# Kernel optimization log

Hardware: AMD Instinct MI355X
Metric: run time of the kernel (lower is better)

Reference implementation:

```python
import jax, jax.numpy as jnp
import numpy as np

NUM_HEADS = 16


def setup_inputs() -> dict:
    key = jax.random.key(0)
    k1, k2, k3, k4 = jax.random.split(key, 4)
    B, S, E = 2, 2048, 1024
    x = jax.random.normal(k1, (B, S, E), dtype=jnp.float32)
    src_padding_mask = jax.random.randint(k2, (B, S), 0, 2) > 0  # True = keep
    # xavier-uniform-ish scale for linear weights (shape (out, in), torch convention)
    w_qkv = jax.random.normal(k3, (3 * E, E), dtype=jnp.float32) * (1.0 / np.sqrt(E))
    w_o = jax.random.normal(k4, (E, E), dtype=jnp.float32) * (1.0 / np.sqrt(E))
    return {"x": x, "src_padding_mask": src_padding_mask, "w_qkv": w_qkv, "w_o": w_o}


def reference(x, src_padding_mask, w_qkv, w_o):
    B, S, E = x.shape
    H = NUM_HEADS
    D = E // H
    # fused qkv projection: (B,S,3E) -> (B,S,H,3D) -> split
    qkv = jnp.einsum("bse,fe->bsf", x, w_qkv).reshape(B, S, H, 3 * D)
    q, k, v = jnp.split(qkv, 3, axis=-1)
    # (B,H,S,D)
    q = q.transpose(0, 2, 1, 3)
    k = k.transpose(0, 2, 1, 3)
    v = v.transpose(0, 2, 1, 3)
    logits = jnp.einsum("bhqd,bhkd->bhqk", q, k) / jnp.sqrt(jnp.float32(D))
    logits = jnp.where(src_padding_mask[:, None, None, :], logits, -jnp.inf)
    attn = jax.nn.softmax(logits, axis=-1)
    values = jnp.einsum("bhqk,bhkd->bhqd", attn, v)  # (B,H,S,D)
    values = values.transpose(0, 2, 1, 3).reshape(B, S, E)
    out = jnp.einsum("bse,fe->bsf", values, w_o)
    return out
```

## Files before the change

kernel.cpp:

```cpp
#include <hip/hip_runtime.h>
#include <hip/hip_bf16.h>

#define B_NUM 2
#define S_LEN 2048
#define E_DIM 1024
#define H_NUM 16
#define D_DIM 64
#define QKV_LD 3072
#define QSCALE_LOG2E 0.18033688011112042f

typedef __attribute__((ext_vector_type(8))) short bf16x8;
typedef __attribute__((ext_vector_type(8))) unsigned short u16x8;
typedef __attribute__((ext_vector_type(4))) unsigned short u16x4;
typedef __attribute__((ext_vector_type(4))) float f32x4;
typedef __attribute__((ext_vector_type(16))) float f32x16;
typedef __attribute__((ext_vector_type(2))) int i32x2;

static __device__ __forceinline__ unsigned short f2bf(float f) {
    union { float f; unsigned int u; } v; v.f = f;
    unsigned int r = v.u + 0x7fffu + ((v.u >> 16) & 1u);
    return (unsigned short)(r >> 16);
}

static __device__ __forceinline__ float bf2f(unsigned short u) {
    union { unsigned int u; float f; } v; v.u = ((unsigned int)u) << 16;
    return v.f;
}

static __device__ __forceinline__ unsigned cvtpk_bf16(float lo, float hi) {
    unsigned r;
    asm("v_cvt_pk_bf16_f32 %0, %1, %2" : "=v"(r) : "v"(lo), "v"(hi));
    return r;
}

static __device__ __forceinline__ void gload16(const void* gsrc, void* ldst) {
    __builtin_amdgcn_global_load_lds(
        (const __attribute__((address_space(1))) unsigned int*)gsrc,
        (__attribute__((address_space(3))) unsigned int*)ldst, 16, 0, 0);
}

__global__ __launch_bounds__(256)
void cvt_f32_bf16(const float* __restrict__ in, unsigned short* __restrict__ outp, int n4) {
    int i = blockIdx.x * blockDim.x + threadIdx.x;
    if (i < n4) {
        float4 f = ((const float4*)in)[i];
        u16x4 o = { f2bf(f.x), f2bf(f.y), f2bf(f.z), f2bf(f.w) };
        ((u16x4*)outp)[i] = o;
    }
}

template <bool OUT_BF16, bool QSCALE>
__global__ __launch_bounds__(256)
void gemm_bt_mfma128(const unsigned short* __restrict__ A,
                     const unsigned short* __restrict__ Bw,
                     void* __restrict__ Cv, int M, int N, int K) {
    __shared__ unsigned short As[128 * 64];
    __shared__ unsigned short Bs[128 * 64];
    char* const AsB = (char*)As;
    char* const BsB = (char*)Bs;
    const int tid  = threadIdx.x;
    const int lane = tid & 63;
    const int w    = tid >> 6;
    const int lg   = lane >> 4;
    const int lq   = lane & 15;
    const int bm = blockIdx.y * 128;
    const int bn = blockIdx.x * 128;
    const int wr = (w >> 1) * 64;
    const int wc = (w & 1) * 64;
    const int lrow8 = lane >> 3;
    const int gblk  = (lane & 7) ^ lrow8;

    f32x4 acc[4][4];
#pragma unroll
    for (int i = 0; i < 4; ++i)
#pragma unroll
        for (int j = 0; j < 4; ++j) acc[i][j] = (f32x4){0.f, 0.f, 0.f, 0.f};

    for (int k0 = 0; k0 < K; k0 += 64) {
        __syncthreads();
#pragma unroll
        for (int t = 0; t < 4; ++t) {
            const int c = w * 4 + t;
            const int row = c * 8 + lrow8;
            gload16(A + (size_t)(bm + row) * K + k0 + gblk * 8, AsB + c * 1024);
            gload16(Bw + (size_t)(bn + row) * K + k0 + gblk * 8, BsB + c * 1024);
        }
        __syncthreads();

        bf16x8 af[4][2], bfr[4][2];
#pragma unroll
        for (int rt = 0; rt < 4; ++rt) {
            const int row = wr + rt * 16 + lq;
            const int sz = (row & 7) << 4;
            af[rt][0] = *(const bf16x8*)(AsB + row * 128 + ((lg * 16)      ^ sz));
            af[rt][1] = *(const bf16x8*)(AsB + row * 128 + ((64 + lg * 16) ^ sz));
        }
#pragma unroll
        for (int ct = 0; ct < 4; ++ct) {
            const int row = wc + ct * 16 + lq;
            const int sz = (row & 7) << 4;
            bfr[ct][0] = *(const bf16x8*)(BsB + row * 128 + ((lg * 16)      ^ sz));
            bfr[ct][1] = *(const bf16x8*)(BsB + row * 128 + ((64 + lg * 16) ^ sz));
        }
#pragma unroll
        for (int rt = 0; rt < 4; ++rt)
#pragma unroll
            for (int ct = 0; ct < 4; ++ct) {
                acc[rt][ct] = __builtin_amdgcn_mfma_f32_16x16x32_bf16(af[rt][0], bfr[ct][0], acc[rt][ct], 0, 0, 0);
                acc[rt][ct] = __builtin_amdgcn_mfma_f32_16x16x32_bf16(af[rt][1], bfr[ct][1], acc[rt][ct], 0, 0, 0);
            }
    }

#pragma unroll
    for (int rt = 0; rt < 4; ++rt)
#pragma unroll
        for (int ct = 0; ct < 4; ++ct) {
            const int row = bm + wr + rt * 16 + lg * 4;
            const int col = bn + wc + ct * 16 + lq;
            float scale = 1.f;
            if constexpr (QSCALE) scale = ((col % 192) < 64) ? QSCALE_LOG2E : 1.f;
#pragma unroll
            for (int r = 0; r < 4; ++r) {
                float vv = acc[rt][ct][r] * scale;
                if constexpr (OUT_BF16)
                    ((unsigned short*)Cv)[(size_t)(row + r) * N + col] = f2bf(vv);
                else
                    ((float*)Cv)[(size_t)(row + r) * N + col] = vv;
            }
        }
}

template <bool OUT_BF16, bool QSCALE>
__global__ __launch_bounds__(256)
void gemm_bt_mfma(const unsigned short* __restrict__ A,
                  const unsigned short* __restrict__ Bw,
                  void* __restrict__ Cv, int M, int N, int K) {
    __shared__ unsigned short As[64 * 64];
    __shared__ unsigned short Bs[64 * 64];
    char* const AsB = (char*)As;
    char* const BsB = (char*)Bs;
    const int tid  = threadIdx.x;
    const int lane = tid & 63;
    const int w    = tid >> 6;
    const int lg   = lane >> 4;
    const int lq   = lane & 15;
    const int bm = blockIdx.y * 64;
    const int bn = blockIdx.x * 64;
    const int wr = (w >> 1) * 32;
    const int wc = (w & 1) * 32;
    const int sr = tid >> 2;
    const int sc = (tid & 3) * 16;
    const int swzS = (sr & 7) << 4;

    f32x4 acc[2][2];
#pragma unroll
    for (int i = 0; i < 2; ++i)
#pragma unroll
        for (int j = 0; j < 2; ++j) acc[i][j] = (f32x4){0.f, 0.f, 0.f, 0.f};

    const unsigned short* ap = A  + (size_t)(bm + sr) * K + sc;
    const unsigned short* bp = Bw + (size_t)(bn + sr) * K + sc;

    for (int k0 = 0; k0 < K; k0 += 64) {
        __syncthreads();
        u16x8 av0 = *(const u16x8*)(ap + k0);
        u16x8 av1 = *(const u16x8*)(ap + k0 + 8);
        u16x8 bv0 = *(const u16x8*)(bp + k0);
        u16x8 bv1 = *(const u16x8*)(bp + k0 + 8);
        *(u16x8*)(AsB + sr * 128 + ((sc * 2)      ^ swzS)) = av0;
        *(u16x8*)(AsB + sr * 128 + ((sc * 2 + 16) ^ swzS)) = av1;
        *(u16x8*)(BsB + sr * 128 + ((sc * 2)      ^ swzS)) = bv0;
        *(u16x8*)(BsB + sr * 128 + ((sc * 2 + 16) ^ swzS)) = bv1;
        __syncthreads();

        bf16x8 af[2][2], bfr[2][2];
#pragma unroll
        for (int rt = 0; rt < 2; ++rt) {
            const int row = wr + rt * 16 + lq;
            const int sz = (row & 7) << 4;
            af[rt][0] = *(const bf16x8*)(AsB + row * 128 + ((lg * 16)      ^ sz));
            af[rt][1] = *(const bf16x8*)(AsB + row * 128 + ((64 + lg * 16) ^ sz));
        }
#pragma unroll
        for (int ct = 0; ct < 2; ++ct) {
            const int row = wc + ct * 16 + lq;
            const int sz = (row & 7) << 4;
            bfr[ct][0] = *(const bf16x8*)(BsB + row * 128 + ((lg * 16)      ^ sz));
            bfr[ct][1] = *(const bf16x8*)(BsB + row * 128 + ((64 + lg * 16) ^ sz));
        }
#pragma unroll
        for (int rt = 0; rt < 2; ++rt)
#pragma unroll
            for (int ct = 0; ct < 2; ++ct) {
                acc[rt][ct] = __builtin_amdgcn_mfma_f32_16x16x32_bf16(af[rt][0], bfr[ct][0], acc[rt][ct], 0, 0, 0);
                acc[rt][ct] = __builtin_amdgcn_mfma_f32_16x16x32_bf16(af[rt][1], bfr[ct][1], acc[rt][ct], 0, 0, 0);
            }
    }

#pragma unroll
    for (int rt = 0; rt < 2; ++rt)
#pragma unroll
        for (int ct = 0; ct < 2; ++ct) {
            const int row = bm + wr + rt * 16 + lg * 4;
            const int col = bn + wc + ct * 16 + lq;
            float scale = 1.f;
            if constexpr (QSCALE) scale = ((col % 192) < 64) ? QSCALE_LOG2E : 1.f;
#pragma unroll
            for (int r = 0; r < 4; ++r) {
                float vv = acc[rt][ct][r] * scale;
                if constexpr (OUT_BF16)
                    ((unsigned short*)Cv)[(size_t)(row + r) * N + col] = f2bf(vv);
                else
                    ((float*)Cv)[(size_t)(row + r) * N + col] = vv;
            }
        }
}

__global__ __launch_bounds__(256)
void attn_v14(const unsigned short* __restrict__ qkv, const int* __restrict__ mask,
              unsigned short* __restrict__ Po, float* __restrict__ Zp) {
    __shared__ __align__(16) char KsP[2][8192];
    __shared__ __align__(16) char VtP[2][8192];
    __shared__ __align__(16) float BiasF[1024];

    const int tid  = threadIdx.x;
    const int lane = tid & 63;
    const int w    = tid >> 6;
    const int ln   = lane & 31;
    const int hi   = lane >> 5;
    const int part = blockIdx.x & 1;
    const int q0   = (blockIdx.x >> 1) * 128;
    const int h  = blockIdx.y;
    const int b  = blockIdx.z;
    const int kvbase = part * 1024;
    const unsigned short* const kv =
        qkv + (size_t)b * S_LEN * QKV_LD + (size_t)h * (3 * D_DIM);

    {
        const int4* mr = (const int4*)(mask + (size_t)b * S_LEN + kvbase);
        int4 m0 = mr[tid];
        float4 f0 = { m0.x ? 0.f : -30000.f, m0.y ? 0.f : -30000.f,
                      m0.z ? 0.f : -30000.f, m0.w ? 0.f : -30000.f };
        ((float4*)BiasF)[tid] = f0;
    }

    bf16x8 qf[4];
    {
        const unsigned short* qp = kv + (size_t)(q0 + w * 32 + ln) * QKV_LD + hi * 8;
#pragma unroll
        for (int kk = 0; kk < 4; ++kk)
            qf[kk] = *(const bf16x8*)(qp + kk * 16);
    }

    const int lrow8 = lane >> 3;
    const int gblk  = (lane & 7) ^ lrow8;
    const int vkb = (tid & 15) * 4;
    const int vdb = (tid >> 4) * 4;

    {
#pragma unroll
        for (int t = 0; t < 2; ++t) {
            const int c = w * 2 + t;
            gload16(kv + (size_t)(kvbase + c * 8 + lrow8) * QKV_LD + D_DIM + gblk * 8,
                    KsP[0] + c * 1024);
        }
        u16x4 vr[4];
#pragma unroll
        for (int i = 0; i < 4; ++i)
            vr[i] = *(const u16x4*)(kv + (size_t)(kvbase + vkb + i) * QKV_LD + 2 * D_DIM + vdb);
#pragma unroll
        for (int j = 0; j < 4; ++j) {
            u16x4 o = { vr[0][j], vr[1][j], vr[2][j], vr[3][j] };
            const int row = vdb + j;
            *(u16x4*)(VtP[0] + row * 128 + ((vkb * 2) ^ ((row & 7) << 4))) = o;
        }
    }
    __syncthreads();

    f32x16 accO[2];
#pragma unroll
    for (int dt = 0; dt < 2; ++dt)
#pragma unroll
        for (int r = 0; r < 16; ++r) accO[dt][r] = 0.f;
    f32x4 rsumv = (f32x4){0.f, 0.f, 0.f, 0.f};

    const int NT = 16;
    for (int it = 0; it < NT; ++it) {
        const int cur = it & 1;
        const int kv0l = it * 64;
        const int kvg  = kvbase + it * 64;
        char* const KsC = KsP[cur];
        char* const VtC = VtP[cur];
        const bool pf = (it + 1 < NT);

        u16x4 vr[4];
        if (pf) {
            const int kvn = kvg + 64;
#pragma unroll
            for (int t = 0; t < 2; ++t) {
                const int c = w * 2 + t;
                gload16(kv + (size_t)(kvn + c * 8 + lrow8) * QKV_LD + D_DIM + gblk * 8,
                        KsP[cur ^ 1] + c * 1024);
            }
#pragma unroll
            for (int i = 0; i < 4; ++i)
                vr[i] = *(const u16x4*)(kv + (size_t)(kvn + vkb + i) * QKV_LD + 2 * D_DIM + vdb);
        }

        f32x16 s[2];
#pragma unroll
        for (int ks = 0; ks < 2; ++ks)
#pragma unroll
            for (int m = 0; m < 4; ++m) {
                f32x4 b4 = *(const f32x4*)(&BiasF[kv0l + ks * 32 + m * 8 + hi * 4]);
#pragma unroll
                for (int i = 0; i < 4; ++i) s[ks][m * 4 + i] = b4[i];
            }
        __builtin_amdgcn_s_setprio(1);
#pragma unroll
        for (int ks = 0; ks < 2; ++ks) {
            const int krow = ks * 32 + ln;
            const int swz = (ln & 7) << 4;
#pragma unroll
            for (int kk = 0; kk < 4; ++kk) {
                bf16x8 kf = *(const bf16x8*)(KsC + krow * 128 + (((kk * 16 + hi * 8) * 2) ^ swz));
                s[ks] = __builtin_amdgcn_mfma_f32_32x32x16_bf16(kf, qf[kk], s[ks], 0, 0, 0);
            }
        }
        __builtin_amdgcn_s_setprio(0);

#pragma unroll
        for (int ks = 0; ks < 2; ++ks)
#pragma unroll
            for (int r = 0; r < 16; ++r) {
                float p = __builtin_amdgcn_exp2f(s[ks][r]);
                s[ks][r] = p;
                rsumv[r & 3] += p;
            }

        bf16x8 pb[4];
#pragma unroll
        for (int ks = 0; ks < 2; ++ks) {
            unsigned wA[4], wB[4];
#pragma unroll
            for (int m = 0; m < 4; ++m) {
                wA[m] = cvtpk_bf16(s[ks][4 * m + 0], s[ks][4 * m + 1]);
                wB[m] = cvtpk_bf16(s[ks][4 * m + 2], s[ks][4 * m + 3]);
            }
#pragma unroll
            for (int t = 0; t < 2; ++t) {
                i32x2 ra = __builtin_amdgcn_permlane32_swap((int)wA[2 * t], (int)wA[2 * t + 1], false, false);
                i32x2 rb = __builtin_amdgcn_permlane32_swap((int)wB[2 * t], (int)wB[2 * t + 1], false, false);
                union { unsigned u[4]; bf16x8 v; } uu;
                uu.u[0] = (unsigned)ra[0];
                uu.u[1] = (unsigned)rb[0];
                uu.u[2] = (unsigned)ra[1];
                uu.u[3] = (unsigned)rb[1];
                pb[ks * 2 + t] = uu.v;
            }
        }

        __builtin_amdgcn_s_setprio(1);
#pragma unroll
        for (int dt = 0; dt < 2; ++dt) {
            const int drow = dt * 32 + ln;
            const int swz = (ln & 7) << 4;
#pragma unroll
            for (int n = 0; n < 4; ++n) {
                bf16x8 va = *(const bf16x8*)(VtC + drow * 128 + (((n * 16 + hi * 8) * 2) ^ swz));
                accO[dt] = __builtin_amdgcn_mfma_f32_32x32x16_bf16(va, pb[n], accO[dt], 0, 0, 0);
            }
        }
        __builtin_amdgcn_s_setprio(0);

        if (pf) {
#pragma unroll
            for (int j = 0; j < 4; ++j) {
                u16x4 o = { vr[0][j], vr[1][j], vr[2][j], vr[3][j] };
                const int row = vdb + j;
                *(u16x4*)(VtP[cur ^ 1] + row * 128 + ((vkb * 2) ^ ((row & 7) << 4))) = o;
            }
        }
        __syncthreads();
    }

    float rsum = rsumv[0] + rsumv[1] + rsumv[2] + rsumv[3];
    {
        i32x2 rr = __builtin_amdgcn_permlane32_swap(__float_as_int(rsum), __float_as_int(rsum), false, false);
        rsum = __int_as_float(rr[0]) + __int_as_float(rr[1]);
    }
    const int q = q0 + w * 32 + ln;
    const float inv = 1.f / rsum;
    unsigned short* po = Po + (((size_t)(part * B_NUM + b) * H_NUM + h) * S_LEN + q) * D_DIM;
#pragma unroll
    for (int dt = 0; dt < 2; ++dt)
#pragma unroll
        for (int m = 0; m < 4; ++m) {
            u16x4 o;
#pragma unroll
            for (int i = 0; i < 4; ++i) o[i] = f2bf(accO[dt][4 * m + i] * inv);
            *(u16x4*)(po + dt * 32 + m * 8 + hi * 4) = o;
        }
    if (hi == 0)
        Zp[((size_t)(part * B_NUM + b) * H_NUM + h) * S_LEN + q] = rsum;
}

__global__ __launch_bounds__(256)
void attn_merge(const unsigned short* __restrict__ Po, const float* __restrict__ Zp,
                unsigned short* __restrict__ vbuf) {
    const int idx = blockIdx.x * 256 + threadIdx.x;
    const int j   = idx & 7;
    const int rh  = idx >> 3;
    const int h   = rh & (H_NUM - 1);
    const int bq  = rh >> 4;
    const int b   = bq >> 11;
    const int q   = bq & (S_LEN - 1);

    const size_t prow0 = ((size_t)(b)          * H_NUM + h) * S_LEN + q;
    const size_t prow1 = ((size_t)(B_NUM + b)  * H_NUM + h) * S_LEN + q;
    const float rs0 = Zp[prow0];
    const float rs1 = Zp[prow1];
    const float is = 1.f / (rs0 + rs1);
    const float w0 = rs0 * is;
    const float w1 = rs1 * is;

    u16x8 a = *(const u16x8*)(Po + prow0 * D_DIM + j * 8);
    u16x8 c = *(const u16x8*)(Po + prow1 * D_DIM + j * 8);
    u16x8 o;
#pragma unroll
    for (int k = 0; k < 8; ++k)
        o[k] = f2bf(bf2f(a[k]) * w0 + bf2f(c[k]) * w1);
    *(u16x8*)(vbuf + (size_t)bq * E_DIM + h * D_DIM + j * 8) = o;
}

extern "C" void kernel_launch(void* const* d_in, const int* in_sizes, int n_in,
                              void* d_out, int out_size, void* d_ws, size_t ws_size,
                              hipStream_t stream) {
    const float* x      = (const float*)d_in[0];
    const int*   mask   = (const int*)d_in[1];
    const float* w_qkv  = (const float*)d_in[2];
    const float* w_o    = (const float*)d_in[3];
    float*       out    = (float*)d_out;

    const int M = B_NUM * S_LEN;
    unsigned short* qkvb = (unsigned short*)d_ws;
    unsigned short* vbuf = qkvb + (size_t)M * 3 * E_DIM;
    unsigned short* xb   = vbuf + (size_t)M * E_DIM;
    unsigned short* wqb  = xb   + (size_t)M * E_DIM;
    unsigned short* wob  = wqb  + (size_t)3 * E_DIM * E_DIM;
    unsigned short* Po   = wob  + (size_t)E_DIM * E_DIM;
    float*          Zp   = (float*)(Po + (size_t)2 * M * E_DIM);

    dim3 blk(256);
    {
        int n4;
        n4 = M * E_DIM / 4;
        cvt_f32_bf16<<<dim3((n4 + 255) / 256), blk, 0, stream>>>(x, xb, n4);
        n4 = 3 * E_DIM * E_DIM / 4;
        cvt_f32_bf16<<<dim3((n4 + 255) / 256), blk, 0, stream>>>(w_qkv, wqb, n4);
        n4 = E_DIM * E_DIM / 4;
        cvt_f32_bf16<<<dim3((n4 + 255) / 256), blk, 0, stream>>>(w_o, wob, n4);
    }

    gemm_bt_mfma128<true, true><<<dim3(3 * E_DIM / 128, M / 128), blk, 0, stream>>>(
        xb, wqb, qkvb, M, 3 * E_DIM, E_DIM);

    attn_v14<<<dim3((S_LEN / 128) * 2, H_NUM, B_NUM), blk, 0, stream>>>(
        qkvb, mask, Po, Zp);

    attn_merge<<<dim3(B_NUM * S_LEN * H_NUM * 8 / 256), blk, 0, stream>>>(Po, Zp, vbuf);

    gemm_bt_mfma<false, false><<<dim3(E_DIM / 64, M / 64), blk, 0, stream>>>(
        vbuf, wob, out, M, E_DIM, E_DIM);
}
```

Baseline: 134.7 us.

## Fold key padding mask into QKV epilogue by zeroing masked K/V rows

Result: no change. 135.5 us (+0.7%).

```diff
diff --git a/kernel.cpp b/kernel.cpp
--- a/kernel.cpp
+++ b/kernel.cpp
@@ -53,7 +53,8 @@
 __global__ __launch_bounds__(256)
 void gemm_bt_mfma128(const unsigned short* __restrict__ A,
                      const unsigned short* __restrict__ Bw,
-                     void* __restrict__ Cv, int M, int N, int K) {
+                     void* __restrict__ Cv, const int* __restrict__ mask,
+                     int M, int N, int K) {
     __shared__ unsigned short As[128 * 64];
     __shared__ unsigned short Bs[128 * 64];
     char* const AsB = (char*)As;
@@ -118,10 +119,17 @@
             const int row = bm + wr + rt * 16 + lg * 4;
             const int col = bn + wc + ct * 16 + lq;
             float scale = 1.f;
-            if constexpr (QSCALE) scale = ((col % 192) < 64) ? QSCALE_LOG2E : 1.f;
+            bool kvcol = false;
+            if constexpr (QSCALE) {
+                scale = ((col % 192) < 64) ? QSCALE_LOG2E : 1.f;
+                kvcol = ((col % 192) >= 64);
+            }
 #pragma unroll
             for (int r = 0; r < 4; ++r) {
                 float vv = acc[rt][ct][r] * scale;
+                if constexpr (QSCALE) {
+                    if (kvcol && mask[row + r] == 0) vv = 0.f;
+                }
                 if constexpr (OUT_BF16)
                     ((unsigned short*)Cv)[(size_t)(row + r) * N + col] = f2bf(vv);
                 else
@@ -130,7 +138,7 @@
         }
 }
 
-template <bool OUT_BF16, bool QSCALE>
+template <bool OUT_BF16>
 __global__ __launch_bounds__(256)
 void gemm_bt_mfma(const unsigned short* __restrict__ A,
                   const unsigned short* __restrict__ Bw,
@@ -203,11 +211,9 @@
         for (int ct = 0; ct < 2; ++ct) {
             const int row = bm + wr + rt * 16 + lg * 4;
             const int col = bn + wc + ct * 16 + lq;
-            float scale = 1.f;
-            if constexpr (QSCALE) scale = ((col % 192) < 64) ? QSCALE_LOG2E : 1.f;
 #pragma unroll
             for (int r = 0; r < 4; ++r) {
-                float vv = acc[rt][ct][r] * scale;
+                float vv = acc[rt][ct][r];
                 if constexpr (OUT_BF16)
                     ((unsigned short*)Cv)[(size_t)(row + r) * N + col] = f2bf(vv);
                 else
@@ -216,12 +222,12 @@
         }
 }
 
-__global__ __launch_bounds__(256)
-void attn_v14(const unsigned short* __restrict__ qkv, const int* __restrict__ mask,
+__global__ __launch_bounds__(256, 4)
+void attn_v15(const unsigned short* __restrict__ qkv, const int* __restrict__ mask,
               unsigned short* __restrict__ Po, float* __restrict__ Zp) {
     __shared__ __align__(16) char KsP[2][8192];
     __shared__ __align__(16) char VtP[2][8192];
-    __shared__ __align__(16) float BiasF[1024];
+    __shared__ float NmLds[4];
 
     const int tid  = threadIdx.x;
     const int lane = tid & 63;
@@ -239,9 +245,10 @@
     {
         const int4* mr = (const int4*)(mask + (size_t)b * S_LEN + kvbase);
         int4 m0 = mr[tid];
-        float4 f0 = { m0.x ? 0.f : -30000.f, m0.y ? 0.f : -30000.f,
-                      m0.z ? 0.f : -30000.f, m0.w ? 0.f : -30000.f };
-        ((float4*)BiasF)[tid] = f0;
+        int cnt = (m0.x == 0) + (m0.y == 0) + (m0.z == 0) + (m0.w == 0);
+#pragma unroll
+        for (int off = 1; off < 64; off <<= 1) cnt += __shfl_xor(cnt, off);
+        if (lane == 0) NmLds[w] = (float)cnt;
     }
 
     bf16x8 qf[4];
@@ -276,6 +283,7 @@
         }
     }
     __syncthreads();
+    const float nmask = NmLds[0] + NmLds[1] + NmLds[2] + NmLds[3];
 
     f32x16 accO[2];
 #pragma unroll
@@ -287,8 +295,7 @@
     const int NT = 16;
     for (int it = 0; it < NT; ++it) {
         const int cur = it & 1;
-        const int kv0l = it * 64;
-        const int kvg  = kvbase + it * 64;
+        const int kvg = kvbase + it * 64;
         char* const KsC = KsP[cur];
         char* const VtC = VtP[cur];
         const bool pf = (it + 1 < NT);
@@ -311,11 +318,7 @@
 #pragma unroll
         for (int ks = 0; ks < 2; ++ks)
 #pragma unroll
-            for (int m = 0; m < 4; ++m) {
-                f32x4 b4 = *(const f32x4*)(&BiasF[kv0l + ks * 32 + m * 8 + hi * 4]);
-#pragma unroll
-                for (int i = 0; i < 4; ++i) s[ks][m * 4 + i] = b4[i];
-            }
+            for (int r = 0; r < 16; ++r) s[ks][r] = 0.f;
         __builtin_amdgcn_s_setprio(1);
 #pragma unroll
         for (int ks = 0; ks < 2; ++ks) {
@@ -389,6 +392,7 @@
         i32x2 rr = __builtin_amdgcn_permlane32_swap(__float_as_int(rsum), __float_as_int(rsum), false, false);
         rsum = __int_as_float(rr[0]) + __int_as_float(rr[1]);
     }
+    rsum -= nmask;
     const int q = q0 + w * 32 + ln;
     const float inv = 1.f / rsum;
     unsigned short* po = Po + (((size_t)(part * B_NUM + b) * H_NUM + h) * S_LEN + q) * D_DIM;
@@ -463,13 +467,13 @@
     }
 
     gemm_bt_mfma128<true, true><<<dim3(3 * E_DIM / 128, M / 128), blk, 0, stream>>>(
-        xb, wqb, qkvb, M, 3 * E_DIM, E_DIM);
-
-    attn_v14<<<dim3((S_LEN / 128) * 2, H_NUM, B_NUM), blk, 0, stream>>>(
+        xb, wqb, qkvb, mask, M, 3 * E_DIM, E_DIM);
+
+    attn_v15<<<dim3((S_LEN / 128) * 2, H_NUM, B_NUM), blk, 0, stream>>>(
         qkvb, mask, Po, Zp);
 
     attn_merge<<<dim3(B_NUM * S_LEN * H_NUM * 8 / 256), blk, 0, stream>>>(Po, Zp, vbuf);
 
-    gemm_bt_mfma<false, false><<<dim3(E_DIM / 64, M / 64), blk, 0, stream>>>(
+    gemm_bt_mfma<false><<<dim3(E_DIM / 64, M / 64), blk, 0, stream>>>(
         vbuf, wob, out, M, E_DIM, E_DIM);
 }
```
